# Kernel optimization log

Measured on AMD Instinct MI355X. Metric: run time of the kernel, lower is better.

## Reference

```python
import jax, jax.numpy as jnp
import numpy as np

HIDDEN = 256

def setup_inputs() -> dict:
    key = jax.random.key(0)
    k1, k2, k3, k4, k5 = jax.random.split(key, 5)
    hidden = jax.random.normal(k1, (1, 32, HIDDEN), dtype=jnp.float32)
    encoder_outputs = jax.random.normal(k2, (32, 8192, HIDDEN), dtype=jnp.float32)
    # nn.Linear(hidden*2, hidden): weight (H, 2H), bias (H,)
    W = jax.random.normal(k3, (HIDDEN, 2 * HIDDEN), dtype=jnp.float32) / np.sqrt(2 * HIDDEN)
    b = jax.random.normal(k4, (HIDDEN,), dtype=jnp.float32) * 0.01
    v = jax.random.uniform(k5, (HIDDEN,), dtype=jnp.float32)
    return {"hidden": hidden, "encoder_outputs": encoder_outputs, "W": W, "b": b, "v": v}

def reference(hidden, encoder_outputs, W, b, v):
    # hidden: (1, B, H) -> (B, 1, H); avoid materializing the concat by
    # splitting Linear(2H->H) into two matmuls (same math as cat + Linear).
    Wh, We = W[:, :HIDDEN], W[:, HIDDEN:]          # each (H, 2H/2)
    h = jnp.transpose(hidden, (1, 0, 2))           # (B, 1, H)
    # (B,1,H)@(H,H)^T broadcasts over seq; (B,S,H)@(H,H)^T
    pre = jnp.einsum('boh,kh->bok', h, Wh) + jnp.einsum('bsh,kh->bsk', encoder_outputs, We) + b
    scores = jnp.tanh(pre)                          # (B, S, H)
    logits = jnp.einsum('bsh,h->bs', scores, v)     # (B, S)
    attn_weights = jax.nn.softmax(logits, axis=1)   # (B, S)
    context = jnp.einsum('bs,bsh->bh', attn_weights, encoder_outputs)  # (B, H)
    return (context, attn_weights)
```

## Files before the change

kernel.cpp:

```cpp
#include <hip/hip_runtime.h>


typedef _Float16 f16x8 __attribute__((ext_vector_type(8)));
typedef float    f32x4 __attribute__((ext_vector_type(4)));

__device__ __forceinline__ float fast_tanh(float x){
  x = fminf(15.f, fmaxf(-15.f, x));
  float e = __expf(2.f * x);
  return (e - 1.f) * __builtin_amdgcn_rcpf(e + 1.f);
}

__device__ __forceinline__ float lane_bcast(float x, int l){
  return __uint_as_float(__builtin_amdgcn_readlane(__float_as_uint(x), l));
}

__global__ void prep_kernel(const float* __restrict__ hidden, const float* __restrict__ W,
                            const float* __restrict__ bias, _Float16* __restrict__ Bfrag,
                            float* __restrict__ qb)
{
  int blk = blockIdx.x;
  if (blk < 256){
    int tid  = blk * 256 + threadIdx.x;
    int j    = tid & 7;
    int lane = (tid >> 3) & 63;
    int kc   = (tid >> 9) & 7;
    int nt   = tid >> 12;
    int lc   = lane & 15, q = lane >> 4;
    int row  = nt * 16 + lc;
    int col  = 256 + kc * 32 + q * 8 + j;
    Bfrag[tid] = (_Float16)W[row * 512 + col];
  } else {
    int b = blk - 256;
    int k = threadIdx.x;
    const float4* hp = (const float4*)(hidden + b * 256);
    const float4* wp = (const float4*)(W + k * 512);
    float s = 0.f;
    for (int i = 0; i < 64; i++){
      float4 h4 = hp[i], w4 = wp[i];
      s += h4.x * w4.x + h4.y * w4.y + h4.z * w4.z + h4.w * w4.w;
    }
    qb[b * 256 + k] = s + bias[k];
  }
}

__global__ __launch_bounds__(1024) void attn_main(
    const float* __restrict__ enc, const _Float16* __restrict__ Bfrag,
    const float* __restrict__ qb, const float* __restrict__ v,
    float* __restrict__ logits, float* __restrict__ P,
    float* __restrict__ mw, float* __restrict__ lw)
{
  __shared__ _Float16 Wf[65536];
  __shared__ float2 qv2[256];

  const int tid = threadIdx.x, wv = tid >> 6, lane = tid & 63;
  const int q = lane >> 4, lc = lane & 15;
  const int b = blockIdx.x >> 3, slab = blockIdx.x & 7;

  {
    const float4* src = (const float4*)Bfrag;
    float4* dst = (float4*)Wf;
    #pragma unroll
    for (int i = 0; i < 8; i++) dst[tid + i * 1024] = src[tid + i * 1024];
    if (tid < 256) qv2[tid] = make_float2(qb[b * 256 + tid], v[tid]);
  }
  __syncthreads();

  const f16x8* Wl = (const f16x8*)Wf;
  const int rowBase0 = b * 8192 + (slab * 32 + wv * 2) * 32;

  f16x8 bf[2][8];
  #define LOAD_BF(base)                                                     \
  {                                                                         \
    const float* er0 = enc + (size_t)((base) + lc) * 256 + q * 8;           \
    _Pragma("unroll")                                                       \
    for (int t = 0; t < 2; t++){                                            \
      const float* er = er0 + t * 16 * 256;                                 \
      _Pragma("unroll")                                                     \
      for (int kc = 0; kc < 8; kc++){                                       \
        float4 x0 = *(const float4*)(er + kc * 32);                         \
        float4 x1 = *(const float4*)(er + kc * 32 + 4);                     \
        f16x8 h;                                                            \
        h[0]=(_Float16)x0.x; h[1]=(_Float16)x0.y;                           \
        h[2]=(_Float16)x0.z; h[3]=(_Float16)x0.w;                           \
        h[4]=(_Float16)x1.x; h[5]=(_Float16)x1.y;                           \
        h[6]=(_Float16)x1.z; h[7]=(_Float16)x1.w;                           \
        bf[t][kc] = h;                                                      \
      }                                                                     \
    }                                                                       \
  }

  LOAD_BF(rowBase0)

  for (int ci = 0; ci < 2; ci++){
    const int rowBase = rowBase0 + ci * 32;
    const int cid = b * 256 + slab * 32 + wv * 2 + ci;

    float lg0 = 0.f, lg1 = 0.f;
    #pragma unroll 2
    for (int nt = 0; nt < 16; nt++){
      f32x4 acc0 = {0, 0, 0, 0}, acc1 = {0, 0, 0, 0};
      #pragma unroll
      for (int kc = 0; kc < 8; kc++){
        f16x8 a = Wl[(nt * 8 + kc) * 64 + lane];
        acc0 = __builtin_amdgcn_mfma_f32_16x16x32_f16(a, bf[0][kc], acc0, 0, 0, 0);
        acc1 = __builtin_amdgcn_mfma_f32_16x16x32_f16(a, bf[1][kc], acc1, 0, 0, 0);
      }
      #pragma unroll
      for (int rr = 0; rr < 4; rr++){
        float2 c = qv2[nt * 16 + q * 4 + rr];
        lg0 += fast_tanh(acc0[rr] + c.x) * c.y;
        lg1 += fast_tanh(acc1[rr] + c.x) * c.y;
      }
    }
    lg0 += __shfl_xor(lg0, 16); lg0 += __shfl_xor(lg0, 32);
    lg1 += __shfl_xor(lg1, 16); lg1 += __shfl_xor(lg1, 32);
    if (q == 0){
      logits[rowBase + lc]      = lg0;
      logits[rowBase + 16 + lc] = lg1;
    }
    float m = fmaxf(lg0, lg1);
    m = fmaxf(m, __shfl_xor(m, 1)); m = fmaxf(m, __shfl_xor(m, 2));
    m = fmaxf(m, __shfl_xor(m, 4)); m = fmaxf(m, __shfl_xor(m, 8));
    float e0 = __expf(lg0 - m), e1 = __expf(lg1 - m);
    float ls = e0 + e1;
    ls += __shfl_xor(ls, 1); ls += __shfl_xor(ls, 2);
    ls += __shfl_xor(ls, 4); ls += __shfl_xor(ls, 8);
    if (lane == 0){ mw[cid] = m; lw[cid] = ls; }

    if (ci == 0) LOAD_BF(rowBase0 + 32)

    float4 ctx = make_float4(0.f, 0.f, 0.f, 0.f);
    const float* ep = enc + (size_t)rowBase * 256 + lane * 4;
    #pragma unroll
    for (int r = 0; r < 16; r++){
      float w0 = lane_bcast(e0, r);
      float w1 = lane_bcast(e1, r);
      float4 a  = *(const float4*)(ep + (size_t)r * 256);
      float4 b4 = *(const float4*)(ep + (size_t)(r + 16) * 256);
      ctx.x += w0 * a.x + w1 * b4.x;
      ctx.y += w0 * a.y + w1 * b4.y;
      ctx.z += w0 * a.z + w1 * b4.z;
      ctx.w += w0 * a.w + w1 * b4.w;
    }
    *(float4*)(P + (size_t)cid * 256 + lane * 4) = ctx;
  }
  #undef LOAD_BF
}

__global__ void attn_finish(const float* __restrict__ logits, const float* __restrict__ P,
                            const float* __restrict__ mw, const float* __restrict__ lw,
                            float* __restrict__ out)
{
  const int b = blockIdx.x >> 1, half = blockIdx.x & 1, t = threadIdx.x;
  __shared__ float se[256], red[8];
  float mv = mw[b * 256 + t], lv = lw[b * 256 + t];
  float m = mv;
  #pragma unroll
  for (int o = 1; o < 64; o <<= 1) m = fmaxf(m, __shfl_xor(m, o));
  if ((t & 63) == 0) red[t >> 6] = m;
  __syncthreads();
  const float M = fmaxf(fmaxf(red[0], red[1]), fmaxf(red[2], red[3]));
  float e = __expf(mv - M);
  se[t] = e;
  float l = e * lv;
  #pragma unroll
  for (int o = 1; o < 64; o <<= 1) l += __shfl_xor(l, o);
  if ((t & 63) == 0) red[4 + (t >> 6)] = l;
  __syncthreads();
  const float L = red[4] + red[5] + red[6] + red[7];
  const float inv = 1.f / L;
  if (half == 0){
    float c0 = 0.f, c1 = 0.f;
    #pragma unroll 8
    for (int ch = 0; ch < 128; ch++){
      c0 += se[ch]       * P[(size_t)(b * 256 + ch) * 256 + t];
      c1 += se[ch + 128] * P[(size_t)(b * 256 + 128 + ch) * 256 + t];
    }
    out[b * 256 + t] = (c0 + c1) * inv;
  }
  const float* lg = logits + (size_t)b * 8192 + half * 4096;
  float* ao = out + 8192 + (size_t)b * 8192 + half * 4096;
  #pragma unroll
  for (int s2 = 0; s2 < 16; s2++) ao[s2 * 256 + t] = __expf(lg[s2 * 256 + t] - M) * inv;
}

extern "C" void kernel_launch(void* const* d_in, const int* in_sizes, int n_in,
                              void* d_out, int out_size, void* d_ws, size_t ws_size,
                              hipStream_t stream)
{
  const float* hidden = (const float*)d_in[0];
  const float* enc    = (const float*)d_in[1];
  const float* W      = (const float*)d_in[2];
  const float* bias   = (const float*)d_in[3];
  const float* v      = (const float*)d_in[4];
  float* out = (float*)d_out;

  char* ws = (char*)d_ws;
  _Float16* Bfrag = (_Float16*)ws;
  float* qb     = (float*)(ws + (128 << 10));
  float* logits = (float*)(ws + (160 << 10));
  float* P      = (float*)(ws + (160 << 10) + (1 << 20));
  float* mw     = (float*)(ws + (160 << 10) + (9 << 20));
  float* lw     = (float*)(ws + (160 << 10) + (9 << 20) + (32 << 10));

  prep_kernel<<<288, 256, 0, stream>>>(hidden, W, bias, Bfrag, qb);
  attn_main<<<256, 1024, 0, stream>>>(enc, Bfrag, qb, v, logits, P, mw, lw);
  attn_finish<<<64, 256, 0, stream>>>(logits, P, mw, lw, out);
}
```

Before: 419.1 us.

## Split context accumulation out of score kernel into separate bandwidth kernel

Moves the weighted context accumulation out of the MFMA score kernel into a new wide-grid kernel that rereads encoder rows using per-chunk softmax weights stored in workspace. The prefetch of the next fragment batch is also moved earlier, right after the MFMA loop. This is meant to shorten the heavy score kernel and get better memory parallelism for the context sum. The cost is an extra kernel launch and a second full pass over the encoder outputs from memory.

```diff
diff --git a/kernel.cpp b/kernel.cpp
--- a/kernel.cpp
+++ b/kernel.cpp
@@ -8,10 +8,6 @@
   x = fminf(15.f, fmaxf(-15.f, x));
   float e = __expf(2.f * x);
   return (e - 1.f) * __builtin_amdgcn_rcpf(e + 1.f);
-}
-
-__device__ __forceinline__ float lane_bcast(float x, int l){
-  return __uint_as_float(__builtin_amdgcn_readlane(__float_as_uint(x), l));
 }
 
 __global__ void prep_kernel(const float* __restrict__ hidden, const float* __restrict__ W,
@@ -43,10 +39,10 @@
   }
 }
 
-__global__ __launch_bounds__(1024) void attn_main(
+__global__ __launch_bounds__(1024) void attn_scores(
     const float* __restrict__ enc, const _Float16* __restrict__ Bfrag,
     const float* __restrict__ qb, const float* __restrict__ v,
-    float* __restrict__ logits, float* __restrict__ P,
+    float* __restrict__ logits, float* __restrict__ swg,
     float* __restrict__ mw, float* __restrict__ lw)
 {
   __shared__ _Float16 Wf[65536];
@@ -112,6 +108,9 @@
         lg1 += fast_tanh(acc1[rr] + c.x) * c.y;
       }
     }
+
+    if (ci == 0) LOAD_BF(rowBase0 + 32)
+
     lg0 += __shfl_xor(lg0, 16); lg0 += __shfl_xor(lg0, 32);
     lg1 += __shfl_xor(lg1, 16); lg1 += __shfl_xor(lg1, 32);
     if (q == 0){
@@ -126,25 +125,25 @@
     ls += __shfl_xor(ls, 1); ls += __shfl_xor(ls, 2);
     ls += __shfl_xor(ls, 4); ls += __shfl_xor(ls, 8);
     if (lane == 0){ mw[cid] = m; lw[cid] = ls; }
-
-    if (ci == 0) LOAD_BF(rowBase0 + 32)
-
-    float4 ctx = make_float4(0.f, 0.f, 0.f, 0.f);
-    const float* ep = enc + (size_t)rowBase * 256 + lane * 4;
-    #pragma unroll
-    for (int r = 0; r < 16; r++){
-      float w0 = lane_bcast(e0, r);
-      float w1 = lane_bcast(e1, r);
-      float4 a  = *(const float4*)(ep + (size_t)r * 256);
-      float4 b4 = *(const float4*)(ep + (size_t)(r + 16) * 256);
-      ctx.x += w0 * a.x + w1 * b4.x;
-      ctx.y += w0 * a.y + w1 * b4.y;
-      ctx.z += w0 * a.z + w1 * b4.z;
-      ctx.w += w0 * a.w + w1 * b4.w;
-    }
-    *(float4*)(P + (size_t)cid * 256 + lane * 4) = ctx;
+    if (q == 0){
+      swg[cid * 32 + lc]      = e0;
+      swg[cid * 32 + 16 + lc] = e1;
+    }
   }
   #undef LOAD_BF
+}
+
+__global__ __launch_bounds__(256) void ctx_kernel(
+    const float* __restrict__ enc, const float* __restrict__ swg,
+    float* __restrict__ P)
+{
+  const int cid = blockIdx.x, t = threadIdx.x;
+  const float* ep = enc + (size_t)cid * 32 * 256 + t;
+  const float* wp = swg + cid * 32;
+  float acc = 0.f;
+  #pragma unroll
+  for (int r = 0; r < 32; r++) acc += wp[r] * ep[(size_t)r * 256];
+  P[(size_t)cid * 256 + t] = acc;
 }
 
 __global__ void attn_finish(const float* __restrict__ logits, const float* __restrict__ P,
@@ -202,8 +201,10 @@
   float* P      = (float*)(ws + (160 << 10) + (1 << 20));
   float* mw     = (float*)(ws + (160 << 10) + (9 << 20));
   float* lw     = (float*)(ws + (160 << 10) + (9 << 20) + (32 << 10));
+  float* swg    = (float*)(ws + (160 << 10) + (9 << 20) + (64 << 10));
 
   prep_kernel<<<288, 256, 0, stream>>>(hidden, W, bias, Bfrag, qb);
-  attn_main<<<256, 1024, 0, stream>>>(enc, Bfrag, qb, v, logits, P, mw, lw);
+  attn_scores<<<256, 1024, 0, stream>>>(enc, Bfrag, qb, v, logits, swg, mw, lw);
+  ctx_kernel<<<8192, 256, 0, stream>>>(enc, swg, P);
   attn_finish<<<64, 256, 0, stream>>>(logits, P, mw, lw, out);
 }
```

After: 450.3 us. +7.5%, slower.

## Use 512-thread blocks and issue encoder loads before W staging to overlap latency

Applied to the files above, without the earlier changes.

Splits attn_main into 512 blocks of 512 threads, so each block covers half as many rows. Encoder rows are now loaded into raw float registers before the shared-memory copy of the W fragments, the conversion to fp16 is deferred, and the second chunk's loads are issued right after the barrier. The MFMA loop also runs at raised wave priority. The goal is to hide global-load latency behind the LDS staging and the compute, at the cost of many more live registers (raw float4 buffers plus two fp16 fragment sets). Each block still stages the full 128KB of W into LDS, so twice as many blocks means twice the total staging traffic.

```diff
diff --git a/kernel.cpp b/kernel.cpp
--- a/kernel.cpp
+++ b/kernel.cpp
@@ -43,7 +43,7 @@
   }
 }
 
-__global__ __launch_bounds__(1024) void attn_main(
+__global__ __launch_bounds__(512) void attn_main(
     const float* __restrict__ enc, const _Float16* __restrict__ Bfrag,
     const float* __restrict__ qb, const float* __restrict__ v,
     float* __restrict__ logits, float* __restrict__ P,
@@ -54,48 +54,61 @@
 
   const int tid = threadIdx.x, wv = tid >> 6, lane = tid & 63;
   const int q = lane >> 4, lc = lane & 15;
-  const int b = blockIdx.x >> 3, slab = blockIdx.x & 7;
+  const int b = blockIdx.x >> 4, slab = blockIdx.x & 15;
+  const int rowBase0 = b * 8192 + slab * 512 + wv * 64;
+
+  float4 pf[2][8][2];
+  f16x8 bfA[2][8], bfB[2][8];
+
+  #define LOAD_RAW(base)                                                    \
+  {                                                                         \
+    _Pragma("unroll")                                                       \
+    for (int t = 0; t < 2; t++){                                            \
+      const float* er = enc + (size_t)((base) + lc + 16 * t) * 256 + q * 8; \
+      _Pragma("unroll")                                                     \
+      for (int kc = 0; kc < 8; kc++){                                       \
+        pf[t][kc][0] = *(const float4*)(er + kc * 32);                      \
+        pf[t][kc][1] = *(const float4*)(er + kc * 32 + 4);                  \
+      }                                                                     \
+    }                                                                       \
+  }
+  #define CVT(bfX)                                                          \
+  {                                                                         \
+    _Pragma("unroll")                                                       \
+    for (int t = 0; t < 2; t++)                                             \
+      _Pragma("unroll")                                                     \
+      for (int kc = 0; kc < 8; kc++){                                       \
+        f16x8 h;                                                            \
+        h[0]=(_Float16)pf[t][kc][0].x; h[1]=(_Float16)pf[t][kc][0].y;       \
+        h[2]=(_Float16)pf[t][kc][0].z; h[3]=(_Float16)pf[t][kc][0].w;       \
+        h[4]=(_Float16)pf[t][kc][1].x; h[5]=(_Float16)pf[t][kc][1].y;       \
+        h[6]=(_Float16)pf[t][kc][1].z; h[7]=(_Float16)pf[t][kc][1].w;       \
+        bfX[t][kc] = h;                                                     \
+      }                                                                     \
+  }
+
+  LOAD_RAW(rowBase0)
 
   {
     const float4* src = (const float4*)Bfrag;
     float4* dst = (float4*)Wf;
     #pragma unroll
-    for (int i = 0; i < 8; i++) dst[tid + i * 1024] = src[tid + i * 1024];
+    for (int i = 0; i < 16; i++) dst[tid + i * 512] = src[tid + i * 512];
     if (tid < 256) qv2[tid] = make_float2(qb[b * 256 + tid], v[tid]);
   }
+  CVT(bfA)
   __syncthreads();
 
+  LOAD_RAW(rowBase0 + 32)
+
   const f16x8* Wl = (const f16x8*)Wf;
-  const int rowBase0 = b * 8192 + (slab * 32 + wv * 2) * 32;
-
-  f16x8 bf[2][8];
-  #define LOAD_BF(base)                                                     \
-  {                                                                         \
-    const float* er0 = enc + (size_t)((base) + lc) * 256 + q * 8;           \
-    _Pragma("unroll")                                                       \
-    for (int t = 0; t < 2; t++){                                            \
-      const float* er = er0 + t * 16 * 256;                                 \
-      _Pragma("unroll")                                                     \
-      for (int kc = 0; kc < 8; kc++){                                       \
-        float4 x0 = *(const float4*)(er + kc * 32);                         \
-        float4 x1 = *(const float4*)(er + kc * 32 + 4);                     \
-        f16x8 h;                                                            \
-        h[0]=(_Float16)x0.x; h[1]=(_Float16)x0.y;                           \
-        h[2]=(_Float16)x0.z; h[3]=(_Float16)x0.w;                           \
-        h[4]=(_Float16)x1.x; h[5]=(_Float16)x1.y;                           \
-        h[6]=(_Float16)x1.z; h[7]=(_Float16)x1.w;                           \
-        bf[t][kc] = h;                                                      \
-      }                                                                     \
-    }                                                                       \
-  }
-
-  LOAD_BF(rowBase0)
-
-  for (int ci = 0; ci < 2; ci++){
+
+  auto compute_chunk = [&](f16x8 (&bf)[2][8], int ci){
     const int rowBase = rowBase0 + ci * 32;
-    const int cid = b * 256 + slab * 32 + wv * 2 + ci;
+    const int cid = b * 256 + slab * 16 + wv * 2 + ci;
 
     float lg0 = 0.f, lg1 = 0.f;
+    __builtin_amdgcn_s_setprio(1);
     #pragma unroll 2
     for (int nt = 0; nt < 16; nt++){
       f32x4 acc0 = {0, 0, 0, 0}, acc1 = {0, 0, 0, 0};
@@ -112,6 +125,10 @@
         lg1 += fast_tanh(acc1[rr] + c.x) * c.y;
       }
     }
+    __builtin_amdgcn_s_setprio(0);
+
+    if (ci == 0) CVT(bfB)
+
     lg0 += __shfl_xor(lg0, 16); lg0 += __shfl_xor(lg0, 32);
     lg1 += __shfl_xor(lg1, 16); lg1 += __shfl_xor(lg1, 32);
     if (q == 0){
@@ -126,8 +143,6 @@
     ls += __shfl_xor(ls, 1); ls += __shfl_xor(ls, 2);
     ls += __shfl_xor(ls, 4); ls += __shfl_xor(ls, 8);
     if (lane == 0){ mw[cid] = m; lw[cid] = ls; }
-
-    if (ci == 0) LOAD_BF(rowBase0 + 32)
 
     float4 ctx = make_float4(0.f, 0.f, 0.f, 0.f);
     const float* ep = enc + (size_t)rowBase * 256 + lane * 4;
@@ -143,8 +158,12 @@
       ctx.w += w0 * a.w + w1 * b4.w;
     }
     *(float4*)(P + (size_t)cid * 256 + lane * 4) = ctx;
-  }
-  #undef LOAD_BF
+  };
+
+  compute_chunk(bfA, 0);
+  compute_chunk(bfB, 1);
+  #undef LOAD_RAW
+  #undef CVT
 }
 
 __global__ void attn_finish(const float* __restrict__ logits, const float* __restrict__ P,
@@ -204,6 +223,6 @@
   float* lw     = (float*)(ws + (160 << 10) + (9 << 20) + (32 << 10));
 
   prep_kernel<<<288, 256, 0, stream>>>(hidden, W, bias, Bfrag, qb);
-  attn_main<<<256, 1024, 0, stream>>>(enc, Bfrag, qb, v, logits, P, mw, lw);
+  attn_main<<<512, 512, 0, stream>>>(enc, Bfrag, qb, v, logits, P, mw, lw);
   attn_finish<<<64, 256, 0, stream>>>(logits, P, mw, lw, out);
 }
```

New measurement: 429.9 us. 2.6% more time.
